# Kernel optimization log

Measured on AMD Instinct MI355X. Metric: run time of the kernel, lower is better.

## Reference

```python
import jax, jax.numpy as jnp
import numpy as np

H = 16
D = 64  # head_dim = 1024 // 16
SCALE = D ** -0.5


def setup_inputs() -> dict:
    key = jax.random.key(0)
    ks = jax.random.split(key, 12)
    B, N, C = 2, 2048, 1024
    s = C ** -0.5
    return {
        "hidden_states": jax.random.normal(ks[0], (B, N, C), jnp.float32),
        "pos_embeds": jax.random.normal(ks[1], (B, N, C), jnp.float32),
        "Wq": jax.random.normal(ks[2], (C, C), jnp.float32) * s,
        "bq": jnp.zeros((C,), jnp.float32),
        "Wk": jax.random.normal(ks[3], (C, C), jnp.float32) * s,
        "bk": jnp.zeros((C,), jnp.float32),
        "Wv": jax.random.normal(ks[4], (C, C), jnp.float32) * s,
        "bv": jnp.zeros((C,), jnp.float32),
        "Wpos": jax.random.normal(ks[5], (C, C), jnp.float32) * s,
        "pos_bias_u": jax.random.normal(ks[6], (H, D), jnp.float32) * 0.1,
        "pos_bias_v": jax.random.normal(ks[7], (H, D), jnp.float32) * 0.1,
        "Wo": jax.random.normal(ks[8], (C, C), jnp.float32) * s,
        "bo": jnp.zeros((C,), jnp.float32),
    }


def reference(hidden_states, pos_embeds, Wq, bq, Wk, bk, Wv, bv, Wpos,
              pos_bias_u, pos_bias_v, Wo, bo):
    B, N, C = hidden_states.shape
    # projections (torch Linear: y = x @ W.T + b), split heads -> (B, N, H, D)
    q = (hidden_states @ Wq.T + bq).reshape(B, N, H, D)
    k = (hidden_states @ Wk.T + bk).reshape(B, N, H, D)
    v = (hidden_states @ Wv.T + bv).reshape(B, N, H, D)
    p = (pos_embeds @ Wpos.T).reshape(B, N, H, D)
    # relative-position biased logits: matrix_ac + matrix_bd
    q_u = q + pos_bias_u  # (B,N,H,D) + (H,D)
    q_v = q + pos_bias_v
    ac = jnp.einsum('bnhd,bmhd->bhnm', q_u, k)
    bd = jnp.einsum('bnhd,bmhd->bhnm', q_v, p)
    attn = jax.nn.softmax((ac + bd) * SCALE, axis=-1)  # (B,H,N,N)
    out = jnp.einsum('bhnm,bmhd->bnhd', attn, v).reshape(B, N, C)
    return out @ Wo.T + bo
```

## Files before the change

### kernel.cpp

```cpp
#include <hip/hip_runtime.h>
#include <hip/hip_bf16.h>


typedef short bf16x8 __attribute__((ext_vector_type(8)));
typedef float f32x4 __attribute__((ext_vector_type(4)));

#define BB 2
#define NN 2048
#define CC 1024
#define HH 16
#define DD 64
#define MM (BB * NN)
#define SC2E 0.18033688f

__device__ __forceinline__ unsigned short f2bf(float f) {
    union { float f; unsigned int u; } x; x.f = f;
    unsigned int r = x.u + 0x7FFFu + ((x.u >> 16) & 1u);
    return (unsigned short)(r >> 16);
}

__device__ __forceinline__ float bf2f(unsigned short s) {
    union { unsigned int u; float f; } x; x.u = ((unsigned int)s) << 16;
    return x.f;
}

__device__ __forceinline__ unsigned int pk2(float a, float b) {
    __hip_bfloat162 h = __float22bfloat162_rn(make_float2(a, b));
    unsigned int u; __builtin_memcpy(&u, &h, 4); return u;
}

typedef __attribute__((address_space(1))) const unsigned int* gas1_t;
typedef __attribute__((address_space(3))) unsigned int* las3_t;

__device__ __forceinline__ void gload_lds16(const unsigned short* g, unsigned short* l) {
    __builtin_amdgcn_global_load_lds((gas1_t)g, (las3_t)l, 16, 0, 0);
}

__global__ __launch_bounds__(256) void cast_f32_bf16(const float* __restrict__ src,
                                                     unsigned short* __restrict__ dst,
                                                     int n4) {
    int i = blockIdx.x * 256 + threadIdx.x;
    if (i >= n4) return;
    float4 v = ((const float4*)src)[i];
    union { unsigned short s[4]; uint2 u; } p;
    p.s[0] = f2bf(v.x); p.s[1] = f2bf(v.y); p.s[2] = f2bf(v.z); p.s[3] = f2bf(v.w);
    ((uint2*)dst)[i] = p.u;
}

template <int MODE>
__global__ __launch_bounds__(256) void gemm_bt(const unsigned short* __restrict__ A,
                                               const unsigned short* __restrict__ B,
                                               void* __restrict__ out0,
                                               const void* __restrict__ aux,
                                               const float* __restrict__ bias) {
    constexpr int K = CC;
    __shared__ unsigned short As[128 * 32];
    __shared__ unsigned short Bs[64 * 32];
    const int t = threadIdx.x;
    const int w = t >> 6, lane = t & 63, l15 = lane & 15, quad = lane >> 4;
    const int m0 = blockIdx.x * 128, n0 = blockIdx.y * 64;
    const int wm = (w >> 1) * 64, wn = (w & 1) * 32;

    f32x4 acc[4][2];
#pragma unroll
    for (int i = 0; i < 4; ++i)
#pragma unroll
        for (int j = 0; j < 2; ++j)
#pragma unroll
            for (int r = 0; r < 4; ++r) acc[i][j][r] = 0.f;

    for (int kb = 0; kb < K; kb += 32) {
        __syncthreads();
#pragma unroll
        for (int j = 0; j < 2; ++j) {
            int id = j * 256 + t;
            int row = id >> 2, c4 = id & 3;
            gload_lds16(&A[(size_t)(m0 + row) * K + kb + c4 * 8], &As[id * 8]);
        }
        {
            int row = t >> 2, c4 = t & 3;
            gload_lds16(&B[(size_t)(n0 + row) * K + kb + c4 * 8], &Bs[t * 8]);
        }
        __syncthreads();
        bf16x8 af[4], bfr[2];
#pragma unroll
        for (int i = 0; i < 4; ++i)
            af[i] = *(const bf16x8*)&As[(wm + i * 16 + l15) * 32 + quad * 8];
#pragma unroll
        for (int j = 0; j < 2; ++j)
            bfr[j] = *(const bf16x8*)&Bs[(wn + j * 16 + l15) * 32 + quad * 8];
#pragma unroll
        for (int i = 0; i < 4; ++i)
#pragma unroll
            for (int j = 0; j < 2; ++j)
                acc[i][j] = __builtin_amdgcn_mfma_f32_16x16x32_bf16(af[i], bfr[j], acc[i][j], 0, 0, 0);
    }

#pragma unroll
    for (int i = 0; i < 4; ++i) {
#pragma unroll
        for (int j = 0; j < 2; ++j) {
            const int col = n0 + wn + j * 16 + l15;
            const int row_base = m0 + wm + i * 16 + quad * 4;
            const float bc = (MODE == 4) ? 0.f : (bias ? bias[col] : 0.f);
            if (MODE == 0) {
#pragma unroll
                for (int r = 0; r < 4; ++r)
                    ((unsigned short*)out0)[(size_t)(row_base + r) * CC + col] = f2bf(acc[i][j][r] + bc);
            } else if (MODE == 1) {
#pragma unroll
                for (int r = 0; r < 4; ++r)
                    ((unsigned short*)out0)[(size_t)(row_base + r) * CC + col] =
                        f2bf((acc[i][j][r] + bc) * SC2E);
            } else if (MODE == 2) {
#pragma unroll
                for (int r = 0; r < 4; ++r)
                    ((float*)out0)[(size_t)(row_base + r) * CC + col] = acc[i][j][r] + bc;
            } else if (MODE == 4) {
#pragma unroll
                for (int r = 0; r < 4; ++r) {
                    float kv = bf2f(((const unsigned short*)aux)[(size_t)(row_base + r) * CC + col]);
                    ((unsigned short*)out0)[(size_t)(row_base + r) * CC + col] = f2bf(acc[i][j][r] + kv);
                }
            } else {
                const int b = row_base >> 11, nseq = row_base & 2047;
                const int hh = col >> 6, dd = col & 63;
                union { unsigned short s[4]; uint2 u; } pk;
#pragma unroll
                for (int r = 0; r < 4; ++r) pk.s[r] = f2bf(acc[i][j][r] + bc);
                size_t idx = ((size_t)(b * HH + hh) * DD + dd) * NN + nseq;
                *(uint2*)&((unsigned short*)out0)[idx] = pk.u;
            }
        }
    }
}

__global__ __launch_bounds__(256) void fuse_c(const unsigned short* __restrict__ k,
                                              const unsigned short* __restrict__ kp,
                                              const float* __restrict__ pbu,
                                              const float* __restrict__ pbv,
                                              float* __restrict__ c) {
    const int gw = (blockIdx.x * 256 + threadIdx.x) >> 6;
    const int lane = threadIdx.x & 63;
    const int row = gw >> 4, h = gw & 15;
    const size_t off = (size_t)row * CC + h * 64 + lane;
    const float u = pbu[h * 64 + lane], v = pbv[h * 64 + lane];
    float val = (u - v) * bf2f(k[off]) + v * bf2f(kp[off]);
#pragma unroll
    for (int o = 1; o < 64; o <<= 1) val += __shfl_xor(val, o);
    if (lane == 0) {
        const int b = row >> 11, n = row & 2047;
        c[((size_t)(b * HH + h)) * NN + n] = val * SC2E;
    }
}

#define PST 80
__global__ __launch_bounds__(256, 2) void attn_kernel(const unsigned short* __restrict__ q,
                                                      const unsigned short* __restrict__ kp,
                                                      const unsigned short* __restrict__ vt,
                                                      const float* __restrict__ cb,
                                                      unsigned short* __restrict__ att) {
    __shared__ unsigned short Ks[64 * 64];
    __shared__ unsigned short Vs[64 * 64];
    __shared__ unsigned short Ps[4][32 * PST];

    const int t = threadIdx.x;
    const int w = t >> 6, lane = t & 63, l15 = lane & 15, quad = lane >> 4;
    const int qt = blockIdx.x, h = blockIdx.y, b = blockIdx.z;
    const int sw = (l15 & 7) * 8;

    bf16x8 qf[2][2];
#pragma unroll
    for (int qb = 0; qb < 2; ++qb) {
        const int qrow = qt * 128 + w * 32 + qb * 16 + l15;
        const size_t qoff = ((size_t)(b * NN + qrow) * HH + h) * DD;
#pragma unroll
        for (int c2 = 0; c2 < 2; ++c2)
            qf[qb][c2] = *(const bf16x8*)&q[qoff + c2 * 32 + quad * 8];
    }

    f32x4 oT[4][2];
    float l_lane[2] = {0.f, 0.f};
#pragma unroll
    for (int db = 0; db < 4; ++db)
#pragma unroll
        for (int qb = 0; qb < 2; ++qb)
#pragma unroll
            for (int r = 0; r < 4; ++r) oT[db][qb][r] = 0.f;

    const size_t kbase = (size_t)b * NN * CC + (size_t)h * DD;
    const size_t vbase = (size_t)(b * HH + h) * DD * NN;
    const size_t cbase = (size_t)(b * HH + h) * NN;

    for (int kt = 0; kt < NN / 64; ++kt) {
        __syncthreads();
#pragma unroll
        for (int j = 0; j < 2; ++j) {
            int id = j * 256 + t, row = id >> 3, c8 = id & 7;
            int gc = (c8 ^ (row & 7)) * 8;
            gload_lds16(&kp[kbase + (size_t)(kt * 64 + row) * CC + gc], &Ks[id * 8]);
            gload_lds16(&vt[vbase + (size_t)row * NN + kt * 64 + gc], &Vs[id * 8]);
        }
        __syncthreads();

        f32x4 s[2][4];
#pragma unroll
        for (int t4 = 0; t4 < 4; ++t4) {
            f32x4 c4 = *(const f32x4*)&cb[cbase + kt * 64 + t4 * 16 + quad * 4];
            s[0][t4] = c4; s[1][t4] = c4;
        }
#pragma unroll
        for (int t4 = 0; t4 < 4; ++t4) {
            const int row = t4 * 16 + l15;
#pragma unroll
            for (int c2 = 0; c2 < 2; ++c2) {
                bf16x8 kf = *(const bf16x8*)&Ks[row * 64 + ((c2 * 4 + quad) * 8 ^ sw)];
#pragma unroll
                for (int qb = 0; qb < 2; ++qb)
                    s[qb][t4] = __builtin_amdgcn_mfma_f32_16x16x32_bf16(kf, qf[qb][c2], s[qb][t4], 0, 0, 0);
            }
        }

#pragma unroll
        for (int qb = 0; qb < 2; ++qb) {
            float rs = 0.f;
#pragma unroll
            for (int t4 = 0; t4 < 4; ++t4)
#pragma unroll
                for (int r = 0; r < 4; ++r) {
                    float pv = exp2f(s[qb][t4][r]);
                    s[qb][t4][r] = pv;
                    rs += pv;
                }
            l_lane[qb] += rs;
#pragma unroll
            for (int t4 = 0; t4 < 4; ++t4) {
                uint2 pk;
                pk.x = pk2(s[qb][t4][0], s[qb][t4][1]);
                pk.y = pk2(s[qb][t4][2], s[qb][t4][3]);
                *(uint2*)&Ps[w][(qb * 16 + l15) * PST + t4 * 16 + quad * 4] = pk;
            }
        }

#pragma unroll
        for (int c2 = 0; c2 < 2; ++c2) {
            bf16x8 pf[2];
#pragma unroll
            for (int qb = 0; qb < 2; ++qb)
                pf[qb] = *(const bf16x8*)&Ps[w][(qb * 16 + l15) * PST + c2 * 32 + quad * 8];
#pragma unroll
            for (int db = 0; db < 4; ++db) {
                bf16x8 vf = *(const bf16x8*)&Vs[(db * 16 + l15) * 64 + ((c2 * 4 + quad) * 8 ^ sw)];
#pragma unroll
                for (int qb = 0; qb < 2; ++qb)
                    oT[db][qb] = __builtin_amdgcn_mfma_f32_16x16x32_bf16(vf, pf[qb], oT[db][qb], 0, 0, 0);
            }
        }
    }

#pragma unroll
    for (int qb = 0; qb < 2; ++qb) {
        float l = l_lane[qb];
        l += __shfl_xor(l, 16);
        l += __shfl_xor(l, 32);
        const float inv = 1.f / l;
        const int qrow = qt * 128 + w * 32 + qb * 16 + l15;
        const size_t ob = ((size_t)(b * NN + qrow) * HH + h) * DD;
#pragma unroll
        for (int db = 0; db < 4; ++db) {
            uint2 pk;
            pk.x = pk2(oT[db][qb][0] * inv, oT[db][qb][1] * inv);
            pk.y = pk2(oT[db][qb][2] * inv, oT[db][qb][3] * inv);
            *(uint2*)&att[ob + db * 16 + quad * 4] = pk;
        }
    }
}

extern "C" void kernel_launch(void* const* d_in, const int* in_sizes, int n_in,
                              void* d_out, int out_size, void* d_ws, size_t ws_size,
                              hipStream_t stream) {
    const float* hs   = (const float*)d_in[0];
    const float* pos  = (const float*)d_in[1];
    const float* Wq   = (const float*)d_in[2];
    const float* bq   = (const float*)d_in[3];
    const float* Wk   = (const float*)d_in[4];
    const float* bk   = (const float*)d_in[5];
    const float* Wv   = (const float*)d_in[6];
    const float* bv   = (const float*)d_in[7];
    const float* Wpos = (const float*)d_in[8];
    const float* pbu  = (const float*)d_in[9];
    const float* pbv  = (const float*)d_in[10];
    const float* Wo   = (const float*)d_in[11];
    const float* bo   = (const float*)d_in[12];
    float* out = (float*)d_out;

    const size_t nHS = (size_t)MM * CC;
    const size_t nW  = (size_t)CC * CC;

    unsigned short* p = (unsigned short*)d_ws;
    unsigned short* hsb  = p;            p += nHS;
    unsigned short* posb = p;            p += nHS;
    unsigned short* wqb  = p;            p += nW;
    unsigned short* wkb  = p;            p += nW;
    unsigned short* wvb  = p;            p += nW;
    unsigned short* wpb  = p;            p += nW;
    unsigned short* wob  = p;            p += nW;
    unsigned short* qsb  = p;            p += nHS;
    unsigned short* kbf  = p;            p += nHS;
    unsigned short* kpb  = p;            p += nHS;
    unsigned short* vtb  = p;            p += nHS;
    float* cb = (float*)p;               p += (size_t)BB * HH * NN * 2;
    unsigned short* attb = hsb;

    cast_f32_bf16<<<(int)(nHS / 4 / 256), 256, 0, stream>>>(hs, hsb, (int)(nHS / 4));
    cast_f32_bf16<<<(int)(nHS / 4 / 256), 256, 0, stream>>>(pos, posb, (int)(nHS / 4));
    cast_f32_bf16<<<(int)(nW / 4 / 256), 256, 0, stream>>>(Wq, wqb, (int)(nW / 4));
    cast_f32_bf16<<<(int)(nW / 4 / 256), 256, 0, stream>>>(Wk, wkb, (int)(nW / 4));
    cast_f32_bf16<<<(int)(nW / 4 / 256), 256, 0, stream>>>(Wv, wvb, (int)(nW / 4));
    cast_f32_bf16<<<(int)(nW / 4 / 256), 256, 0, stream>>>(Wpos, wpb, (int)(nW / 4));
    cast_f32_bf16<<<(int)(nW / 4 / 256), 256, 0, stream>>>(Wo, wob, (int)(nW / 4));

    dim3 ggrid(MM / 128, CC / 64);
    gemm_bt<1><<<ggrid, 256, 0, stream>>>(hsb, wqb, qsb, nullptr, bq);
    gemm_bt<0><<<ggrid, 256, 0, stream>>>(hsb, wkb, kbf, nullptr, bk);
    gemm_bt<3><<<ggrid, 256, 0, stream>>>(hsb, wvb, vtb, nullptr, bv);
    gemm_bt<4><<<ggrid, 256, 0, stream>>>(posb, wpb, kpb, kbf, nullptr);

    fuse_c<<<MM * HH / 4, 256, 0, stream>>>(kbf, kpb, pbu, pbv, cb);

    dim3 agrid(NN / 128, HH, BB);
    attn_kernel<<<agrid, 256, 0, stream>>>(qsb, kpb, vtb, cb, attb);

    gemm_bt<2><<<ggrid, 256, 0, stream>>>(attb, wob, out, nullptr, bo);
}
```

Baseline: 301.5 us.

## Double-buffer LDS tiles in GEMM and attention, merge cast launches

The GEMM and attention kernels now keep two shared-memory buffers for their operand tiles. Each iteration issues the asynchronous global-to-LDS loads for the next tile before computing on the current one, so only one barrier per iteration remains. This is meant to hide global load latency behind MFMA work, at the cost of twice the LDS footprint, which could reduce occupancy. The seven separate fp32-to-bf16 cast launches are also merged into one 2D-grid kernel that uses a packed conversion intrinsic, cutting launch overhead.

```diff
diff --git a/kernel.cpp b/kernel.cpp
--- a/kernel.cpp
+++ b/kernel.cpp
@@ -36,15 +36,20 @@
     __builtin_amdgcn_global_load_lds((gas1_t)g, (las3_t)l, 16, 0, 0);
 }
 
-__global__ __launch_bounds__(256) void cast_f32_bf16(const float* __restrict__ src,
-                                                     unsigned short* __restrict__ dst,
-                                                     int n4) {
-    int i = blockIdx.x * 256 + threadIdx.x;
-    if (i >= n4) return;
-    float4 v = ((const float4*)src)[i];
-    union { unsigned short s[4]; uint2 u; } p;
-    p.s[0] = f2bf(v.x); p.s[1] = f2bf(v.y); p.s[2] = f2bf(v.z); p.s[3] = f2bf(v.w);
-    ((uint2*)dst)[i] = p.u;
+struct CastArgs {
+    const float* src[7];
+    unsigned short* dst[7];
+    int n4[7];
+};
+__global__ __launch_bounds__(256) void cast_all(CastArgs a) {
+    const int seg = blockIdx.y;
+    const int i = blockIdx.x * 256 + threadIdx.x;
+    if (i >= a.n4[seg]) return;
+    float4 v = ((const float4*)a.src[seg])[i];
+    uint2 u;
+    u.x = pk2(v.x, v.y);
+    u.y = pk2(v.z, v.w);
+    ((uint2*)a.dst[seg])[i] = u;
 }
 
 template <int MODE>
@@ -54,13 +59,17 @@
                                                const void* __restrict__ aux,
                                                const float* __restrict__ bias) {
     constexpr int K = CC;
-    __shared__ unsigned short As[128 * 32];
-    __shared__ unsigned short Bs[64 * 32];
+    __shared__ unsigned short As[2][128 * 32];
+    __shared__ unsigned short Bs[2][64 * 32];
     const int t = threadIdx.x;
     const int w = t >> 6, lane = t & 63, l15 = lane & 15, quad = lane >> 4;
     const int m0 = blockIdx.x * 128, n0 = blockIdx.y * 64;
     const int wm = (w >> 1) * 64, wn = (w & 1) * 32;
 
+    const int ar0 = t >> 2, ac = (t & 3) * 8;
+    const int ar1 = 64 + ar0;
+    const int br = t >> 2, bc = (t & 3) * 8;
+
     f32x4 acc[4][2];
 #pragma unroll
     for (int i = 0; i < 4; ++i)
@@ -69,26 +78,26 @@
 #pragma unroll
             for (int r = 0; r < 4; ++r) acc[i][j][r] = 0.f;
 
-    for (int kb = 0; kb < K; kb += 32) {
+    gload_lds16(&A[(size_t)(m0 + ar0) * K + ac], &As[0][t * 8]);
+    gload_lds16(&A[(size_t)(m0 + ar1) * K + ac], &As[0][(256 + t) * 8]);
+    gload_lds16(&B[(size_t)(n0 + br) * K + bc], &Bs[0][t * 8]);
+
+    for (int kb = 0; kb < K / 32; ++kb) {
         __syncthreads();
-#pragma unroll
-        for (int j = 0; j < 2; ++j) {
-            int id = j * 256 + t;
-            int row = id >> 2, c4 = id & 3;
-            gload_lds16(&A[(size_t)(m0 + row) * K + kb + c4 * 8], &As[id * 8]);
-        }
-        {
-            int row = t >> 2, c4 = t & 3;
-            gload_lds16(&B[(size_t)(n0 + row) * K + kb + c4 * 8], &Bs[t * 8]);
-        }
-        __syncthreads();
+        const int cur = kb & 1;
+        if (kb + 1 < K / 32) {
+            const int nb = cur ^ 1, ko = (kb + 1) * 32;
+            gload_lds16(&A[(size_t)(m0 + ar0) * K + ko + ac], &As[nb][t * 8]);
+            gload_lds16(&A[(size_t)(m0 + ar1) * K + ko + ac], &As[nb][(256 + t) * 8]);
+            gload_lds16(&B[(size_t)(n0 + br) * K + ko + bc], &Bs[nb][t * 8]);
+        }
         bf16x8 af[4], bfr[2];
 #pragma unroll
         for (int i = 0; i < 4; ++i)
-            af[i] = *(const bf16x8*)&As[(wm + i * 16 + l15) * 32 + quad * 8];
+            af[i] = *(const bf16x8*)&As[cur][(wm + i * 16 + l15) * 32 + quad * 8];
 #pragma unroll
         for (int j = 0; j < 2; ++j)
-            bfr[j] = *(const bf16x8*)&Bs[(wn + j * 16 + l15) * 32 + quad * 8];
+            bfr[j] = *(const bf16x8*)&Bs[cur][(wn + j * 16 + l15) * 32 + quad * 8];
 #pragma unroll
         for (int i = 0; i < 4; ++i)
 #pragma unroll
@@ -102,20 +111,20 @@
         for (int j = 0; j < 2; ++j) {
             const int col = n0 + wn + j * 16 + l15;
             const int row_base = m0 + wm + i * 16 + quad * 4;
-            const float bc = (MODE == 4) ? 0.f : (bias ? bias[col] : 0.f);
+            const float bc2 = (MODE == 4) ? 0.f : (bias ? bias[col] : 0.f);
             if (MODE == 0) {
 #pragma unroll
                 for (int r = 0; r < 4; ++r)
-                    ((unsigned short*)out0)[(size_t)(row_base + r) * CC + col] = f2bf(acc[i][j][r] + bc);
+                    ((unsigned short*)out0)[(size_t)(row_base + r) * CC + col] = f2bf(acc[i][j][r] + bc2);
             } else if (MODE == 1) {
 #pragma unroll
                 for (int r = 0; r < 4; ++r)
                     ((unsigned short*)out0)[(size_t)(row_base + r) * CC + col] =
-                        f2bf((acc[i][j][r] + bc) * SC2E);
+                        f2bf((acc[i][j][r] + bc2) * SC2E);
             } else if (MODE == 2) {
 #pragma unroll
                 for (int r = 0; r < 4; ++r)
-                    ((float*)out0)[(size_t)(row_base + r) * CC + col] = acc[i][j][r] + bc;
+                    ((float*)out0)[(size_t)(row_base + r) * CC + col] = acc[i][j][r] + bc2;
             } else if (MODE == 4) {
 #pragma unroll
                 for (int r = 0; r < 4; ++r) {
@@ -127,7 +136,7 @@
                 const int hh = col >> 6, dd = col & 63;
                 union { unsigned short s[4]; uint2 u; } pk;
 #pragma unroll
-                for (int r = 0; r < 4; ++r) pk.s[r] = f2bf(acc[i][j][r] + bc);
+                for (int r = 0; r < 4; ++r) pk.s[r] = f2bf(acc[i][j][r] + bc2);
                 size_t idx = ((size_t)(b * HH + hh) * DD + dd) * NN + nseq;
                 *(uint2*)&((unsigned short*)out0)[idx] = pk.u;
             }
@@ -160,8 +169,8 @@
                                                       const unsigned short* __restrict__ vt,
                                                       const float* __restrict__ cb,
                                                       unsigned short* __restrict__ att) {
-    __shared__ unsigned short Ks[64 * 64];
-    __shared__ unsigned short Vs[64 * 64];
+    __shared__ unsigned short Ks[2][64 * 64];
+    __shared__ unsigned short Vs[2][64 * 64];
     __shared__ unsigned short Ps[4][32 * PST];
 
     const int t = threadIdx.x;
@@ -169,6 +178,13 @@
     const int qt = blockIdx.x, h = blockIdx.y, b = blockIdx.z;
     const int sw = (l15 & 7) * 8;
 
+    const size_t kbase = (size_t)b * NN * CC + (size_t)h * DD;
+    const size_t vbase = (size_t)(b * HH + h) * DD * NN;
+    const size_t cbase = (size_t)(b * HH + h) * NN;
+
+    const int sr0 = t >> 3, sc0 = ((t & 7) ^ (sr0 & 7)) * 8;
+    const int sr1 = 32 + (t >> 3), sc1 = ((t & 7) ^ (sr1 & 7)) * 8;
+
     bf16x8 qf[2][2];
 #pragma unroll
     for (int qb = 0; qb < 2; ++qb) {
@@ -188,20 +204,22 @@
 #pragma unroll
             for (int r = 0; r < 4; ++r) oT[db][qb][r] = 0.f;
 
-    const size_t kbase = (size_t)b * NN * CC + (size_t)h * DD;
-    const size_t vbase = (size_t)(b * HH + h) * DD * NN;
-    const size_t cbase = (size_t)(b * HH + h) * NN;
+    gload_lds16(&kp[kbase + (size_t)sr0 * CC + sc0], &Ks[0][t * 8]);
+    gload_lds16(&kp[kbase + (size_t)sr1 * CC + sc1], &Ks[0][(256 + t) * 8]);
+    gload_lds16(&vt[vbase + (size_t)sr0 * NN + sc0], &Vs[0][t * 8]);
+    gload_lds16(&vt[vbase + (size_t)sr1 * NN + sc1], &Vs[0][(256 + t) * 8]);
 
     for (int kt = 0; kt < NN / 64; ++kt) {
         __syncthreads();
-#pragma unroll
-        for (int j = 0; j < 2; ++j) {
-            int id = j * 256 + t, row = id >> 3, c8 = id & 7;
-            int gc = (c8 ^ (row & 7)) * 8;
-            gload_lds16(&kp[kbase + (size_t)(kt * 64 + row) * CC + gc], &Ks[id * 8]);
-            gload_lds16(&vt[vbase + (size_t)row * NN + kt * 64 + gc], &Vs[id * 8]);
-        }
-        __syncthreads();
+        const int cur = kt & 1;
+        if (kt + 1 < NN / 64) {
+            const int nb = cur ^ 1;
+            const size_t ko = (size_t)(kt + 1) * 64;
+            gload_lds16(&kp[kbase + (ko + sr0) * CC + sc0], &Ks[nb][t * 8]);
+            gload_lds16(&kp[kbase + (ko + sr1) * CC + sc1], &Ks[nb][(256 + t) * 8]);
+            gload_lds16(&vt[vbase + (size_t)sr0 * NN + ko + sc0], &Vs[nb][t * 8]);
+            gload_lds16(&vt[vbase + (size_t)sr1 * NN + ko + sc1], &Vs[nb][(256 + t) * 8]);
+        }
 
         f32x4 s[2][4];
 #pragma unroll
@@ -214,7 +232,7 @@
             const int row = t4 * 16 + l15;
 #pragma unroll
             for (int c2 = 0; c2 < 2; ++c2) {
-                bf16x8 kf = *(const bf16x8*)&Ks[row * 64 + ((c2 * 4 + quad) * 8 ^ sw)];
+                bf16x8 kf = *(const bf16x8*)&Ks[cur][row * 64 + ((c2 * 4 + quad) * 8 ^ sw)];
 #pragma unroll
                 for (int qb = 0; qb < 2; ++qb)
                     s[qb][t4] = __builtin_amdgcn_mfma_f32_16x16x32_bf16(kf, qf[qb][c2], s[qb][t4], 0, 0, 0);
@@ -250,7 +268,7 @@
                 pf[qb] = *(const bf16x8*)&Ps[w][(qb * 16 + l15) * PST + c2 * 32 + quad * 8];
 #pragma unroll
             for (int db = 0; db < 4; ++db) {
-                bf16x8 vf = *(const bf16x8*)&Vs[(db * 16 + l15) * 64 + ((c2 * 4 + quad) * 8 ^ sw)];
+                bf16x8 vf = *(const bf16x8*)&Vs[cur][(db * 16 + l15) * 64 + ((c2 * 4 + quad) * 8 ^ sw)];
 #pragma unroll
                 for (int qb = 0; qb < 2; ++qb)
                     oT[db][qb] = __builtin_amdgcn_mfma_f32_16x16x32_bf16(vf, pf[qb], oT[db][qb], 0, 0, 0);
@@ -312,13 +330,16 @@
     float* cb = (float*)p;               p += (size_t)BB * HH * NN * 2;
     unsigned short* attb = hsb;
 
-    cast_f32_bf16<<<(int)(nHS / 4 / 256), 256, 0, stream>>>(hs, hsb, (int)(nHS / 4));
-    cast_f32_bf16<<<(int)(nHS / 4 / 256), 256, 0, stream>>>(pos, posb, (int)(nHS / 4));
-    cast_f32_bf16<<<(int)(nW / 4 / 256), 256, 0, stream>>>(Wq, wqb, (int)(nW / 4));
-    cast_f32_bf16<<<(int)(nW / 4 / 256), 256, 0, stream>>>(Wk, wkb, (int)(nW / 4));
-    cast_f32_bf16<<<(int)(nW / 4 / 256), 256, 0, stream>>>(Wv, wvb, (int)(nW / 4));
-    cast_f32_bf16<<<(int)(nW / 4 / 256), 256, 0, stream>>>(Wpos, wpb, (int)(nW / 4));
-    cast_f32_bf16<<<(int)(nW / 4 / 256), 256, 0, stream>>>(Wo, wob, (int)(nW / 4));
+    CastArgs ca;
+    ca.src[0] = hs;   ca.dst[0] = hsb;  ca.n4[0] = (int)(nHS / 4);
+    ca.src[1] = pos;  ca.dst[1] = posb; ca.n4[1] = (int)(nHS / 4);
+    ca.src[2] = Wq;   ca.dst[2] = wqb;  ca.n4[2] = (int)(nW / 4);
+    ca.src[3] = Wk;   ca.dst[3] = wkb;  ca.n4[3] = (int)(nW / 4);
+    ca.src[4] = Wv;   ca.dst[4] = wvb;  ca.n4[4] = (int)(nW / 4);
+    ca.src[5] = Wpos; ca.dst[5] = wpb;  ca.n4[5] = (int)(nW / 4);
+    ca.src[6] = Wo;   ca.dst[6] = wob;  ca.n4[6] = (int)(nW / 4);
+    dim3 cgrid((unsigned)(nHS / 4 / 256), 7);
+    cast_all<<<cgrid, 256, 0, stream>>>(ca);
 
     dim3 ggrid(MM / 128, CC / 64);
     gemm_bt<1><<<ggrid, 256, 0, stream>>>(hsb, wqb, qsb, nullptr, bq);
```

Result: slower. 317.8 us (+5.4%).
